# Optimization experiments

Measured on AMD Instinct MI355X. Metric: run time of the kernel, lower is better.

Reference implementation:

```python
import jax, jax.numpy as jnp
import numpy as np

N, E, D, H, G, C = 100000, 1200000, 64, 64, 128, 10


def setup_inputs() -> dict:
    key = jax.random.key(0)
    ks = jax.random.split(key, 20)
    def lin(k, fin, fout):
        kw, kb = jax.random.split(k)
        s = 1.0 / np.sqrt(fin)
        return (jax.random.uniform(kw, (fin, fout), jnp.float32, -s, s),
                jax.random.uniform(kb, (fout,), jnp.float32, -s, s))
    w1a, b1a = lin(ks[0], D, H)
    w1b, b1b = lin(ks[1], H, H)
    w2a, b2a = lin(ks[2], H, H)
    w2b, b2b = lin(ks[3], H, H)
    w3a, b3a = lin(ks[4], H, H)
    w3b, b3b = lin(ks[5], H, H)
    wc, bc = lin(ks[6], H, C)
    x = jax.random.normal(ks[7], (N, D), jnp.float32)
    edge_index = jax.random.randint(ks[8], (2, E), 0, N, dtype=jnp.int32)
    batch = jnp.sort(jax.random.randint(ks[9], (N,), 0, G, dtype=jnp.int32))
    return {"x": x, "w1a": w1a, "b1a": b1a, "w1b": w1b, "b1b": b1b,
            "w2a": w2a, "b2a": b2a, "w2b": w2b, "b2b": b2b,
            "w3a": w3a, "b3a": b3a, "w3b": w3b, "b3b": b3b,
            "wc": wc, "bc": bc, "edge_index": edge_index, "batch": batch}


def _gin_layer(x, src, dst, wa, ba, wb, bb):
    # GINConv (eps=0): mlp(x + sum_{j in N(i)} x_j), then outer ReLU from GIN.forward
    agg = jax.ops.segment_sum(x[src], dst, num_segments=N)  # [N, d]
    h = x + agg
    h = jax.nn.relu(h @ wa + ba) @ wb + bb
    return jax.nn.relu(h)


def reference(x, w1a, b1a, w1b, b1b, w2a, b2a, w2b, b2b,
              w3a, b3a, w3b, b3b, wc, bc, edge_index, batch):
    src, dst = edge_index[0], edge_index[1]
    x = _gin_layer(x, src, dst, w1a, b1a, w1b, b1b)
    x = _gin_layer(x, src, dst, w2a, b2a, w2b, b2b)
    x = _gin_layer(x, src, dst, w3a, b3a, w3b, b3b)
    # global mean pool over graphs
    sums = jax.ops.segment_sum(x, batch, num_segments=G)              # [G, H]
    cnts = jax.ops.segment_sum(jnp.ones((N,), x.dtype), batch, num_segments=G)
    pooled = sums / jnp.maximum(cnts, 1.0)[:, None]
    return pooled @ wc + bc  # [G, C]
```

## Files before the change

### kernel.cpp

```cpp
#include <hip/hip_runtime.h>
#include <hip/hip_bf16.h>


#define N_NODES 100000
#define N_EDGES 1200000
#define N_GRAPH 128
#define N_CLS   10
#define NBUCK   391
#define BCAP    4096
#define BSH     12

typedef __bf16 bf16_t;
typedef __bf16 bf16x8 __attribute__((ext_vector_type(8)));
typedef float  f32x4  __attribute__((ext_vector_type(4)));

__global__ void tobf_kernel(const float* __restrict__ x, bf16_t* __restrict__ xb,
                            int* __restrict__ bcnt, float* __restrict__ gsum,
                            const float* __restrict__ w1a, const float* __restrict__ w1b,
                            const float* __restrict__ w2a, const float* __restrict__ w2b,
                            const float* __restrict__ w3a, const float* __restrict__ w3b,
                            bf16_t* __restrict__ wfragG,
                            bf16_t* __restrict__ hPad, bf16_t* __restrict__ xAPad) {
    const int tid = threadIdx.x;
    if (blockIdx.x == 0) {
        for (int i = tid; i < NBUCK; i += 256) bcnt[i] = 0;
    } else if (blockIdx.x == 1) {
        f32x4* g4 = (f32x4*)gsum;
        for (int i = tid; i < N_GRAPH * 16; i += 256)
            g4[i] = (f32x4){0.f, 0.f, 0.f, 0.f};
        if (tid < 64) {
            xb[N_NODES * 64 + tid]    = (bf16_t)0.f;
            hPad[N_NODES * 64 + tid]  = (bf16_t)0.f;
            xAPad[N_NODES * 64 + tid] = (bf16_t)0.f;
        }
    } else if (blockIdx.x <= 4) {
        const int L = blockIdx.x - 2;
        const float* wA = L == 0 ? w1a : (L == 1 ? w2a : w3a);
        const float* wB = L == 0 ? w1b : (L == 1 ? w2b : w3b);
        const int k  = tid >> 2;
        const int n0 = (tid & 3) << 4;
        const int ks = k >> 5, qd = (k >> 3) & 3, jj = k & 7;
        const int fi = ((n0 >> 4) << 1) + ks;
#pragma unroll
        for (int m = 0; m < 2; ++m) {
            const float* w = m ? wB : wA;
            const f32x4 v0 = *(const f32x4*)(w + k * 64 + n0);
            const f32x4 v1 = *(const f32x4*)(w + k * 64 + n0 + 4);
            const f32x4 v2 = *(const f32x4*)(w + k * 64 + n0 + 8);
            const f32x4 v3 = *(const f32x4*)(w + k * 64 + n0 + 12);
            bf16_t* dst = wfragG + ((L * 2 + m) * 8 + fi) * 512 + jj;
#pragma unroll
            for (int l = 0; l < 4; ++l) {
                dst[(qd * 16 + l) * 8]      = (bf16_t)v0[l];
                dst[(qd * 16 + 4 + l) * 8]  = (bf16_t)v1[l];
                dst[(qd * 16 + 8 + l) * 8]  = (bf16_t)v2[l];
                dst[(qd * 16 + 12 + l) * 8] = (bf16_t)v3[l];
            }
        }
    }
    const int i = (blockIdx.x * 256 + tid) * 8;
    const f32x4 a = *(const f32x4*)(x + i);
    const f32x4 b = *(const f32x4*)(x + i + 4);
    bf16x8 o;
#pragma unroll
    for (int j = 0; j < 4; ++j) { o[j] = (bf16_t)a[j]; o[4 + j] = (bf16_t)b[j]; }
    *(bf16x8*)(xb + i) = o;
}

__global__ void binA_kernel(const int* __restrict__ ei,
                            int* __restrict__ bcnt,
                            int* __restrict__ bpair) {
    __shared__ int lcnt[NBUCK];
    __shared__ int lbase[NBUCK];
    const int t = threadIdx.x;
    for (int b = t; b < NBUCK; b += 256) lcnt[b] = 0;
    __syncthreads();
    const int e0 = (blockIdx.x * 256 + t) * 4;
    int4 s4, d4; int b[4], r[4];
    const bool valid = e0 < N_EDGES;
    if (valid) {
        s4 = *(const int4*)(ei + e0);
        d4 = *(const int4*)(ei + N_EDGES + e0);
        b[0] = d4.x >> 8; b[1] = d4.y >> 8; b[2] = d4.z >> 8; b[3] = d4.w >> 8;
        r[0] = atomicAdd(&lcnt[b[0]], 1);
        r[1] = atomicAdd(&lcnt[b[1]], 1);
        r[2] = atomicAdd(&lcnt[b[2]], 1);
        r[3] = atomicAdd(&lcnt[b[3]], 1);
    }
    __syncthreads();
    for (int bb = t; bb < NBUCK; bb += 256) {
        const int c = lcnt[bb];
        lbase[bb] = c ? atomicAdd(&bcnt[bb], c) : 0;
    }
    __syncthreads();
    if (valid) {
        const int ss[4] = {s4.x, s4.y, s4.z, s4.w};
        const int dd[4] = {d4.x, d4.y, d4.z, d4.w};
#pragma unroll
        for (int j = 0; j < 4; ++j) {
            const int slot = lbase[b[j]] + r[j];
            if (slot < BCAP)
                bpair[(b[j] << BSH) + slot] = (ss[j] << 8) | (dd[j] & 255);
        }
    }
}

__global__ void sortfill_kernel(const int* __restrict__ bpair,
                                const int* __restrict__ bcnt,
                                int* __restrict__ offset, int* __restrict__ csr) {
    __shared__ int red[256];
    __shared__ int hist[256];
    __shared__ int l[256];
    __shared__ int cursor[256];
    const int b = blockIdx.x;
    const int t = threadIdx.x;
    const int base = b << BSH;

    int part = 0;
    for (int i = t; i < b; i += 256) {
        int c = bcnt[i];
        part += (c < BCAP ? c : BCAP);
    }
    red[t] = part;
    __syncthreads();
    for (int d = 128; d > 0; d >>= 1) {
        if (t < d) red[t] += red[t + d];
        __syncthreads();
    }
    const int cbase = red[0];
    int cnt = bcnt[b];
    cnt = cnt < BCAP ? cnt : BCAP;
    if (b == NBUCK - 1 && t == 0) offset[N_NODES] = cbase + cnt;
    __syncthreads();

    hist[t] = 0;
    __syncthreads();
    for (int i = t; i < cnt; i += 256)
        atomicAdd(&hist[bpair[base + i] & 255], 1);
    __syncthreads();

    const int v = hist[t];
    l[t] = v;
    __syncthreads();
    for (int d = 1; d < 256; d <<= 1) {
        int u = l[t];
        if (t >= d) u += l[t - d];
        __syncthreads();
        l[t] = u;
        __syncthreads();
    }
    const int gpos = cbase + l[t] - v;
    const int node = (b << 8) + t;
    if (node < N_NODES) offset[node] = gpos;
    cursor[t] = gpos;
    __syncthreads();

    for (int i = t; i < cnt; i += 256) {
        const int p = bpair[base + i];
        const int pos = atomicAdd(&cursor[p & 255], 1);
        csr[pos] = p >> 8;
    }
}

#define G8(S, J, ACC)                                                          \
    {                                                                          \
        const int t0 = __shfl(S, (J) + 0), t1 = __shfl(S, (J) + 1);            \
        const int t2 = __shfl(S, (J) + 2), t3 = __shfl(S, (J) + 3);            \
        const int t4 = __shfl(S, (J) + 4), t5 = __shfl(S, (J) + 5);            \
        const int t6 = __shfl(S, (J) + 6), t7 = __shfl(S, (J) + 7);            \
        const float u0 = (float)x[t0 * 64 + f], u1 = (float)x[t1 * 64 + f];    \
        const float u2 = (float)x[t2 * 64 + f], u3 = (float)x[t3 * 64 + f];    \
        const float u4 = (float)x[t4 * 64 + f], u5 = (float)x[t5 * 64 + f];    \
        const float u6 = (float)x[t6 * 64 + f], u7 = (float)x[t7 * 64 + f];    \
        ACC += ((u0 + u1) + (u2 + u3)) + ((u4 + u5) + (u6 + u7));              \
    }

#define ROWPAIR(I, SA, CA, DA, OA, SB, CB, DB, OB)                             \
    {                                                                          \
        float accA = (float)x[(r0w + I) * 64 + f];                             \
        float accB = (float)x[(r0w + I + 4) * 64 + f];                         \
        const int cmax = (CA) > (CB) ? (CA) : (CB);                            \
        for (int j = 0; j < cmax; j += 8) {                                    \
            if (j < (CA)) { G8(SA, j, accA) }                                  \
            if (j < (CB)) { G8(SB, j, accB) }                                  \
        }                                                                      \
        if ((DA) > 64 || (DB) > 64) {                      \
            for (int base = 64; base < (DA) || base < (DB); base += 64) {      \
                const int ra = (DA) - base, rb2 = (DB) - base;                 \
                const int ca2 = ra <= 0 ? 0 : (ra < 64 ? ra : 64);             \
                const int cb2 = rb2 <= 0 ? 0 : (rb2 < 64 ? rb2 : 64);          \
                int sA2 = N_NODES, sB2 = N_NODES;                              \
                if (f < ca2) sA2 = csr[(OA) + base + f];                       \
                if (f < cb2) sB2 = csr[(OB) + base + f];                       \
                const int cm2 = ca2 > cb2 ? ca2 : cb2;                         \
                for (int j = 0; j < cm2; j += 8) {                             \
                    if (j < ca2) { G8(sA2, j, accA) }                          \
                    if (j < cb2) { G8(sB2, j, accB) }                          \
                }                                                              \
            }                                                                  \
        }                                                                      \
        hs[half * 8 + I][lane]     = (bf16_t)accA;                             \
        hs[half * 8 + I + 4][lane] = (bf16_t)accB;                             \
    }

template <int POOL>
__global__ void gmlp_kernel(const bf16_t* __restrict__ x,
                            const int* __restrict__ offset,
                            const int* __restrict__ csr,
                            const bf16_t* __restrict__ wf,
                            const float* __restrict__ ba, const float* __restrict__ bb,
                            bf16_t* __restrict__ xout,
                            const int* __restrict__ batch,
                            float* __restrict__ gsum) {
    __shared__ __align__(16) bf16_t hs[16][72];
    __shared__ __align__(16) bf16_t h2[16][72];

    const int tid  = threadIdx.x;
    const int half = tid >> 6;
    const int lane = tid & 63;
    const int l15  = lane & 15;
    const int quad = lane >> 4;

    const int rb  = blockIdx.x * 16;
    const int r0w = rb + half * 8;
    const int f   = lane;

    int offv = 0;
    if (lane < 9) offv = offset[r0w + lane];
    const int o0 = __shfl(offv, 0), o1 = __shfl(offv, 1), o2 = __shfl(offv, 2);
    const int o3 = __shfl(offv, 3), o4 = __shfl(offv, 4), o5 = __shfl(offv, 5);
    const int o6 = __shfl(offv, 6), o7 = __shfl(offv, 7), o8 = __shfl(offv, 8);
    const int d0 = o1 - o0, d1 = o2 - o1, d2 = o3 - o2, d3 = o4 - o3;
    const int d4 = o5 - o4, d5 = o6 - o5, d6 = o7 - o6, d7 = o8 - o7;
    const int c0 = d0 < 64 ? d0 : 64, c1 = d1 < 64 ? d1 : 64;
    const int c2 = d2 < 64 ? d2 : 64, c3 = d3 < 64 ? d3 : 64;
    const int c4 = d4 < 64 ? d4 : 64, c5 = d5 < 64 ? d5 : 64;
    const int c6 = d6 < 64 ? d6 : 64, c7 = d7 < 64 ? d7 : 64;

    int s0 = N_NODES, s1 = N_NODES, s2 = N_NODES, s3 = N_NODES;
    int s4 = N_NODES, s5 = N_NODES, s6 = N_NODES, s7 = N_NODES;
    if (f < c0) s0 = csr[o0 + f];
    if (f < c1) s1 = csr[o1 + f];
    if (f < c2) s2 = csr[o2 + f];
    if (f < c3) s3 = csr[o3 + f];
    if (f < c4) s4 = csr[o4 + f];
    if (f < c5) s5 = csr[o5 + f];
    if (f < c6) s6 = csr[o6 + f];
    if (f < c7) s7 = csr[o7 + f];

    ROWPAIR(0, s0, c0, d0, o0, s4, c4, d4, o4)
    ROWPAIR(1, s1, c1, d1, o1, s5, c5, d5, o5)
    ROWPAIR(2, s2, c2, d2, o2, s6, c6, d6, o6)
    ROWPAIR(3, s3, c3, d3, o3, s7, c7, d7, o7)

    __syncthreads();

    {
        bf16x8 af[2];
#pragma unroll
        for (int ks = 0; ks < 2; ++ks)
            af[ks] = *(const bf16x8*)(&hs[l15][ks * 32 + quad * 8]);
#pragma unroll
        for (int c = 0; c < 2; ++c) {
            const int ct = half * 2 + c;
            const bf16x8 b0 = *(const bf16x8*)(wf + (0 * 8 + ct * 2 + 0) * 512 + lane * 8);
            const bf16x8 b1 = *(const bf16x8*)(wf + (0 * 8 + ct * 2 + 1) * 512 + lane * 8);
            f32x4 acc = {0.f, 0.f, 0.f, 0.f};
            acc = __builtin_amdgcn_mfma_f32_16x16x32_bf16(af[0], b0, acc, 0, 0, 0);
            acc = __builtin_amdgcn_mfma_f32_16x16x32_bf16(af[1], b1, acc, 0, 0, 0);
            const float bv = ba[ct * 16 + l15];
#pragma unroll
            for (int r = 0; r < 4; ++r) {
                float h = acc[r] + bv;
                h = h > 0.f ? h : 0.f;
                h2[quad * 4 + r][ct * 16 + l15] = (bf16_t)h;
            }
        }
    }

    __syncthreads();

    {
        bf16x8 a2[2];
#pragma unroll
        for (int ks = 0; ks < 2; ++ks)
            a2[ks] = *(const bf16x8*)(&h2[l15][ks * 32 + quad * 8]);
#pragma unroll
        for (int c = 0; c < 2; ++c) {
            const int ct = half * 2 + c;
            const bf16x8 b0 = *(const bf16x8*)(wf + (1 * 8 + ct * 2 + 0) * 512 + lane * 8);
            const bf16x8 b1 = *(const bf16x8*)(wf + (1 * 8 + ct * 2 + 1) * 512 + lane * 8);
            f32x4 acc = {0.f, 0.f, 0.f, 0.f};
            acc = __builtin_amdgcn_mfma_f32_16x16x32_bf16(a2[0], b0, acc, 0, 0, 0);
            acc = __builtin_amdgcn_mfma_f32_16x16x32_bf16(a2[1], b1, acc, 0, 0, 0);
            const float bv = bb[ct * 16 + l15];
#pragma unroll
            for (int r = 0; r < 4; ++r) {
                float h = acc[r] + bv;
                h = h > 0.f ? h : 0.f;
                hs[quad * 4 + r][ct * 16 + l15] = (bf16_t)h;
            }
        }
    }

    __syncthreads();

    if (POOL) {
        int cur = -1;
        float acc = 0.f;
        for (int r = 0; r < 8; ++r) {
            const int row = r0w + r;
            const int g = batch[row];
            const float v = (float)hs[half * 8 + r][lane];
            if (g != cur) {
                if (cur >= 0) unsafeAtomicAdd(gsum + cur * 64 + lane, acc);
                acc = 0.f;
                cur = g;
            }
            acc += v;
        }
        if (cur >= 0) unsafeAtomicAdd(gsum + cur * 64 + lane, acc);
    } else {
        const int row16 = half * 8 + (lane >> 3);
        const int colg  = (lane & 7) * 8;
        const bf16x8 v = *(const bf16x8*)&hs[row16][colg];
        *(bf16x8*)(xout + (rb + row16) * 64 + colg) = v;
    }
}

__global__ void cls_kernel(const float* __restrict__ gsum,
                           const int* __restrict__ batch,
                           const float* __restrict__ wc, const float* __restrict__ bc,
                           float* __restrict__ out) {
    const int g = blockIdx.x;
    const int c = threadIdx.x;
    if (c >= N_CLS) return;
    int lo = 0, hi = N_NODES;
    while (lo < hi) { const int m = (lo + hi) >> 1; if (batch[m] < g) lo = m + 1; else hi = m; }
    const int lb = lo;
    lo = 0; hi = N_NODES;
    while (lo < hi) { const int m = (lo + hi) >> 1; if (batch[m] <= g) lo = m + 1; else hi = m; }
    const int cnt = lo - lb;
    const float inv = 1.f / (float)(cnt > 1 ? cnt : 1);
    float acc = bc[c];
    for (int k = 0; k < 64; ++k)
        acc += gsum[g * 64 + k] * inv * wc[k * N_CLS + c];
    out[g * N_CLS + c] = acc;
}

extern "C" void kernel_launch(void* const* d_in, const int* in_sizes, int n_in,
                              void* d_out, int out_size, void* d_ws, size_t ws_size,
                              hipStream_t stream) {
    const float* x   = (const float*)d_in[0];
    const float* w1a = (const float*)d_in[1];
    const float* b1a = (const float*)d_in[2];
    const float* w1b = (const float*)d_in[3];
    const float* b1b = (const float*)d_in[4];
    const float* w2a = (const float*)d_in[5];
    const float* b2a = (const float*)d_in[6];
    const float* w2b = (const float*)d_in[7];
    const float* b2b = (const float*)d_in[8];
    const float* w3a = (const float*)d_in[9];
    const float* b3a = (const float*)d_in[10];
    const float* w3b = (const float*)d_in[11];
    const float* b3b = (const float*)d_in[12];
    const float* wc  = (const float*)d_in[13];
    const float* bc  = (const float*)d_in[14];
    const int*   ei    = (const int*)d_in[15];
    const int*   batch = (const int*)d_in[16];
    float* out = (float*)d_out;

    char*   ws     = (char*)d_ws;
    int*    bcnt   = (int*)ws;
    int*    offset = (int*)(ws + 3136);
    int*    csr    = (int*)(ws + 403152);
    int*    bpair  = (int*)(ws + 5203152);
    bf16_t* xbf    = (bf16_t*)(ws + 11609296);
    bf16_t* h      = (bf16_t*)(ws + 24409424);
    bf16_t* xA     = (bf16_t*)(ws + 37209552);
    float*  gsum   = (float*)(ws + 50009680);
    bf16_t* wfragG = (bf16_t*)(ws + 50042448);

    const int e4grid = (N_EDGES / 4 + 255) / 256;
    const int tiles  = N_NODES / 16;

    tobf_kernel<<<(N_NODES * 64) / (256 * 8), 256, 0, stream>>>(
        x, xbf, bcnt, gsum, w1a, w1b, w2a, w2b, w3a, w3b, wfragG, h, xA);

    binA_kernel<<<e4grid, 256, 0, stream>>>(ei, bcnt, bpair);
    sortfill_kernel<<<NBUCK, 256, 0, stream>>>(bpair, bcnt, offset, csr);

    gmlp_kernel<0><<<tiles, 128, 0, stream>>>(xbf, offset, csr, wfragG,         b1a, b1b, xA, nullptr, nullptr);
    gmlp_kernel<0><<<tiles, 128, 0, stream>>>(xA,  offset, csr, wfragG + 8192,  b2a, b2b, h,  nullptr, nullptr);
    gmlp_kernel<1><<<tiles, 128, 0, stream>>>(h,   offset, csr, wfragG + 16384, b3a, b3b, nullptr, batch, gsum);

    cls_kernel<<<N_GRAPH, 64, 0, stream>>>(gsum, batch, wc, bc, out);
}
```

Measured before the change: 287.7 us.

## Process two 16-row tiles per block and prefetch second tile's CSR during GEMMs

Each gmlp block now handles 32 rows as two sequential 16-row tiles. The second tile's offsets and first-chunk CSR neighbor indices are loaded while the first tile's MLP GEMMs run, so that index-load latency overlaps compute. The grid is halved, which reduces parallelism and occupancy slack for latency hiding, and the preloaded indices add register pressure.

New measurement: 329.3 us. 14.4% more time.

```diff
diff --git a/kernel.cpp b/kernel.cpp
--- a/kernel.cpp
+++ b/kernel.cpp
@@ -175,23 +175,40 @@
         ACC += ((u0 + u1) + (u2 + u3)) + ((u4 + u5) + (u6 + u7));              \
     }
 
-#define ROWPAIR(I, SA, CA, DA, OA, SB, CB, DB, OB)                             \
+#define PRELOAD1(OV, X, SX)                                                    \
     {                                                                          \
-        float accA = (float)x[(r0w + I) * 64 + f];                             \
-        float accB = (float)x[(r0w + I + 4) * 64 + f];                         \
-        const int cmax = (CA) > (CB) ? (CA) : (CB);                            \
+        const int o_ = __shfl(OV, X);                                          \
+        const int d_ = __shfl(OV, (X) + 1) - o_;                               \
+        const int c_ = d_ < 64 ? d_ : 64;                                      \
+        SX = N_NODES;                                                          \
+        if (f < c_) SX = csr[o_ + f];                                          \
+    }
+#define PRELOAD8(OV, S0_, S1_, S2_, S3_, S4_, S5_, S6_, S7_)                   \
+    PRELOAD1(OV, 0, S0_) PRELOAD1(OV, 1, S1_) PRELOAD1(OV, 2, S2_)             \
+    PRELOAD1(OV, 3, S3_) PRELOAD1(OV, 4, S4_) PRELOAD1(OV, 5, S5_)             \
+    PRELOAD1(OV, 6, S6_) PRELOAD1(OV, 7, S7_)
+
+#define ROWPAIR(I, OV, SA, SB, R0W)                                            \
+    {                                                                          \
+        const int oA = __shfl(OV, I),     eA = __shfl(OV, (I) + 1);            \
+        const int oB = __shfl(OV, (I) + 4), eB = __shfl(OV, (I) + 5);          \
+        const int dA = eA - oA, dB = eB - oB;                                  \
+        const int cA = dA < 64 ? dA : 64, cB = dB < 64 ? dB : 64;              \
+        float accA = (float)x[((R0W) + I) * 64 + f];                           \
+        float accB = (float)x[((R0W) + I + 4) * 64 + f];                       \
+        const int cmax = cA > cB ? cA : cB;                                    \
         for (int j = 0; j < cmax; j += 8) {                                    \
-            if (j < (CA)) { G8(SA, j, accA) }                                  \
-            if (j < (CB)) { G8(SB, j, accB) }                                  \
+            if (j < cA) { G8(SA, j, accA) }                                    \
+            if (j < cB) { G8(SB, j, accB) }                                    \
         }                                                                      \
-        if ((DA) > 64 || (DB) > 64) {                      \
-            for (int base = 64; base < (DA) || base < (DB); base += 64) {      \
-                const int ra = (DA) - base, rb2 = (DB) - base;                 \
+        if (dA > 64 || dB > 64) {                          \
+            for (int base = 64; base < dA || base < dB; base += 64) {          \
+                const int ra = dA - base, rb2 = dB - base;                     \
                 const int ca2 = ra <= 0 ? 0 : (ra < 64 ? ra : 64);             \
                 const int cb2 = rb2 <= 0 ? 0 : (rb2 < 64 ? rb2 : 64);          \
                 int sA2 = N_NODES, sB2 = N_NODES;                              \
-                if (f < ca2) sA2 = csr[(OA) + base + f];                       \
-                if (f < cb2) sB2 = csr[(OB) + base + f];                       \
+                if (f < ca2) sA2 = csr[oA + base + f];                         \
+                if (f < cb2) sB2 = csr[oB + base + f];                         \
                 const int cm2 = ca2 > cb2 ? ca2 : cb2;                         \
                 for (int j = 0; j < cm2; j += 8) {                             \
                     if (j < ca2) { G8(sA2, j, accA) }                          \
@@ -201,6 +218,77 @@
         }                                                                      \
         hs[half * 8 + I][lane]     = (bf16_t)accA;                             \
         hs[half * 8 + I + 4][lane] = (bf16_t)accB;                             \
+    }
+
+#define GEMM1_BODY                                                             \
+    {                                                                          \
+        bf16x8 af[2];                                                          \
+        _Pragma("unroll")                                                      \
+        for (int ks = 0; ks < 2; ++ks)                                         \
+            af[ks] = *(const bf16x8*)(&hs[l15][ks * 32 + quad * 8]);           \
+        _Pragma("unroll")                                                      \
+        for (int c = 0; c < 2; ++c) {                                          \
+            const int ct = half * 2 + c;                                       \
+            const bf16x8 b0 = *(const bf16x8*)(wf + (ct * 2 + 0) * 512 + lane * 8); \
+            const bf16x8 b1 = *(const bf16x8*)(wf + (ct * 2 + 1) * 512 + lane * 8); \
+            f32x4 acc = {0.f, 0.f, 0.f, 0.f};                                  \
+            acc = __builtin_amdgcn_mfma_f32_16x16x32_bf16(af[0], b0, acc, 0, 0, 0); \
+            acc = __builtin_amdgcn_mfma_f32_16x16x32_bf16(af[1], b1, acc, 0, 0, 0); \
+            const float bv = ba[ct * 16 + l15];                                \
+            _Pragma("unroll")                                                  \
+            for (int r = 0; r < 4; ++r) {                                      \
+                float h = acc[r] + bv;                                         \
+                h = h > 0.f ? h : 0.f;                                         \
+                h2[quad * 4 + r][ct * 16 + l15] = (bf16_t)h;                   \
+            }                                                                  \
+        }                                                                      \
+    }
+
+#define GEMM2_BODY                                                             \
+    {                                                                          \
+        bf16x8 a2[2];                                                          \
+        _Pragma("unroll")                                                      \
+        for (int ks = 0; ks < 2; ++ks)                                         \
+            a2[ks] = *(const bf16x8*)(&h2[l15][ks * 32 + quad * 8]);           \
+        _Pragma("unroll")                                                      \
+        for (int c = 0; c < 2; ++c) {                                          \
+            const int ct = half * 2 + c;                                       \
+            const bf16x8 b0 = *(const bf16x8*)(wf + (8 + ct * 2 + 0) * 512 + lane * 8); \
+            const bf16x8 b1 = *(const bf16x8*)(wf + (8 + ct * 2 + 1) * 512 + lane * 8); \
+            f32x4 acc = {0.f, 0.f, 0.f, 0.f};                                  \
+            acc = __builtin_amdgcn_mfma_f32_16x16x32_bf16(a2[0], b0, acc, 0, 0, 0); \
+            acc = __builtin_amdgcn_mfma_f32_16x16x32_bf16(a2[1], b1, acc, 0, 0, 0); \
+            const float bv = bb[ct * 16 + l15];                                \
+            _Pragma("unroll")                                                  \
+            for (int r = 0; r < 4; ++r) {                                      \
+                float h = acc[r] + bv;                                         \
+                h = h > 0.f ? h : 0.f;                                         \
+                hs[quad * 4 + r][ct * 16 + l15] = (bf16_t)h;                   \
+            }                                                                  \
+        }                                                                      \
+    }
+
+#define EPILOGUE(RB, R0W)                                                      \
+    if (POOL) {                                                                \
+        int cur = -1;                                                          \
+        float acc = 0.f;                                                       \
+        for (int r = 0; r < 8; ++r) {                                          \
+            const int row = (R0W) + r;                                         \
+            const int g = batch[row];                        \
+            const float v = (float)hs[half * 8 + r][lane];                     \
+            if (g != cur) {                                                    \
+                if (cur >= 0) unsafeAtomicAdd(gsum + cur * 64 + lane, acc);    \
+                acc = 0.f;                                                     \
+                cur = g;                                                       \
+            }                                                                  \
+            acc += v;                                                          \
+        }                                                                      \
+        if (cur >= 0) unsafeAtomicAdd(gsum + cur * 64 + lane, acc);            \
+    } else {                                                                   \
+        const int row16 = half * 8 + (lane >> 3);                              \
+        const int colg  = (lane & 7) * 8;                                      \
+        const bf16x8 v = *(const bf16x8*)&hs[row16][colg];                     \
+        *(bf16x8*)(xout + ((RB) + row16) * 64 + colg) = v;                     \
     }
 
 template <int POOL>
@@ -220,112 +308,50 @@
     const int lane = tid & 63;
     const int l15  = lane & 15;
     const int quad = lane >> 4;
-
-    const int rb  = blockIdx.x * 16;
-    const int r0w = rb + half * 8;
-    const int f   = lane;
-
-    int offv = 0;
-    if (lane < 9) offv = offset[r0w + lane];
-    const int o0 = __shfl(offv, 0), o1 = __shfl(offv, 1), o2 = __shfl(offv, 2);
-    const int o3 = __shfl(offv, 3), o4 = __shfl(offv, 4), o5 = __shfl(offv, 5);
-    const int o6 = __shfl(offv, 6), o7 = __shfl(offv, 7), o8 = __shfl(offv, 8);
-    const int d0 = o1 - o0, d1 = o2 - o1, d2 = o3 - o2, d3 = o4 - o3;
-    const int d4 = o5 - o4, d5 = o6 - o5, d6 = o7 - o6, d7 = o8 - o7;
-    const int c0 = d0 < 64 ? d0 : 64, c1 = d1 < 64 ? d1 : 64;
-    const int c2 = d2 < 64 ? d2 : 64, c3 = d3 < 64 ? d3 : 64;
-    const int c4 = d4 < 64 ? d4 : 64, c5 = d5 < 64 ? d5 : 64;
-    const int c6 = d6 < 64 ? d6 : 64, c7 = d7 < 64 ? d7 : 64;
-
-    int s0 = N_NODES, s1 = N_NODES, s2 = N_NODES, s3 = N_NODES;
-    int s4 = N_NODES, s5 = N_NODES, s6 = N_NODES, s7 = N_NODES;
-    if (f < c0) s0 = csr[o0 + f];
-    if (f < c1) s1 = csr[o1 + f];
-    if (f < c2) s2 = csr[o2 + f];
-    if (f < c3) s3 = csr[o3 + f];
-    if (f < c4) s4 = csr[o4 + f];
-    if (f < c5) s5 = csr[o5 + f];
-    if (f < c6) s6 = csr[o6 + f];
-    if (f < c7) s7 = csr[o7 + f];
-
-    ROWPAIR(0, s0, c0, d0, o0, s4, c4, d4, o4)
-    ROWPAIR(1, s1, c1, d1, o1, s5, c5, d5, o5)
-    ROWPAIR(2, s2, c2, d2, o2, s6, c6, d6, o6)
-    ROWPAIR(3, s3, c3, d3, o3, s7, c7, d7, o7)
-
-    __syncthreads();
-
-    {
-        bf16x8 af[2];
-#pragma unroll
-        for (int ks = 0; ks < 2; ++ks)
-            af[ks] = *(const bf16x8*)(&hs[l15][ks * 32 + quad * 8]);
-#pragma unroll
-        for (int c = 0; c < 2; ++c) {
-            const int ct = half * 2 + c;
-            const bf16x8 b0 = *(const bf16x8*)(wf + (0 * 8 + ct * 2 + 0) * 512 + lane * 8);
-            const bf16x8 b1 = *(const bf16x8*)(wf + (0 * 8 + ct * 2 + 1) * 512 + lane * 8);
-            f32x4 acc = {0.f, 0.f, 0.f, 0.f};
-            acc = __builtin_amdgcn_mfma_f32_16x16x32_bf16(af[0], b0, acc, 0, 0, 0);
-            acc = __builtin_amdgcn_mfma_f32_16x16x32_bf16(af[1], b1, acc, 0, 0, 0);
-            const float bv = ba[ct * 16 + l15];
-#pragma unroll
-            for (int r = 0; r < 4; ++r) {
-                float h = acc[r] + bv;
-                h = h > 0.f ? h : 0.f;
-                h2[quad * 4 + r][ct * 16 + l15] = (bf16_t)h;
-            }
-        }
-    }
-
-    __syncthreads();
-
-    {
-        bf16x8 a2[2];
-#pragma unroll
-        for (int ks = 0; ks < 2; ++ks)
-            a2[ks] = *(const bf16x8*)(&h2[l15][ks * 32 + quad * 8]);
-#pragma unroll
-        for (int c = 0; c < 2; ++c) {
-            const int ct = half * 2 + c;
-            const bf16x8 b0 = *(const bf16x8*)(wf + (1 * 8 + ct * 2 + 0) * 512 + lane * 8);
-            const bf16x8 b1 = *(const bf16x8*)(wf + (1 * 8 + ct * 2 + 1) * 512 + lane * 8);
-            f32x4 acc = {0.f, 0.f, 0.f, 0.f};
-            acc = __builtin_amdgcn_mfma_f32_16x16x32_bf16(a2[0], b0, acc, 0, 0, 0);
-            acc = __builtin_amdgcn_mfma_f32_16x16x32_bf16(a2[1], b1, acc, 0, 0, 0);
-            const float bv = bb[ct * 16 + l15];
-#pragma unroll
-            for (int r = 0; r < 4; ++r) {
-                float h = acc[r] + bv;
-                h = h > 0.f ? h : 0.f;
-                hs[quad * 4 + r][ct * 16 + l15] = (bf16_t)h;
-            }
-        }
-    }
-
-    __syncthreads();
-
-    if (POOL) {
-        int cur = -1;
-        float acc = 0.f;
-        for (int r = 0; r < 8; ++r) {
-            const int row = r0w + r;
-            const int g = batch[row];
-            const float v = (float)hs[half * 8 + r][lane];
-            if (g != cur) {
-                if (cur >= 0) unsafeAtomicAdd(gsum + cur * 64 + lane, acc);
-                acc = 0.f;
-                cur = g;
-            }
-            acc += v;
-        }
-        if (cur >= 0) unsafeAtomicAdd(gsum + cur * 64 + lane, acc);
-    } else {
-        const int row16 = half * 8 + (lane >> 3);
-        const int colg  = (lane & 7) * 8;
-        const bf16x8 v = *(const bf16x8*)&hs[row16][colg];
-        *(bf16x8*)(xout + (rb + row16) * 64 + colg) = v;
-    }
+    const int f    = lane;
+
+    const int rb0  = blockIdx.x * 32;
+    const int rb1  = rb0 + 16;
+    const int r0wA = rb0 + half * 8;
+    const int r0wB = rb1 + half * 8;
+
+    int offvA = 0;
+    if (lane < 9) offvA = offset[r0wA + lane];
+    int a0, a1, a2, a3, a4, a5, a6, a7;
+    PRELOAD8(offvA, a0, a1, a2, a3, a4, a5, a6, a7)
+
+    ROWPAIR(0, offvA, a0, a4, r0wA)
+    ROWPAIR(1, offvA, a1, a5, r0wA)
+    ROWPAIR(2, offvA, a2, a6, r0wA)
+    ROWPAIR(3, offvA, a3, a7, r0wA)
+
+    int offvB = 0;
+    if (lane < 9) offvB = offset[r0wB + lane];
+
+    __syncthreads();
+    GEMM1_BODY
+
+    int b0_, b1_, b2_, b3_, b4_, b5_, b6_, b7_;
+    PRELOAD8(offvB, b0_, b1_, b2_, b3_, b4_, b5_, b6_, b7_)
+
+    __syncthreads();
+    GEMM2_BODY
+    __syncthreads();
+    EPILOGUE(rb0, r0wA)
+
+    __syncthreads();
+
+    ROWPAIR(0, offvB, b0_, b4_, r0wB)
+    ROWPAIR(1, offvB, b1_, b5_, r0wB)
+    ROWPAIR(2, offvB, b2_, b6_, r0wB)
+    ROWPAIR(3, offvB, b3_, b7_, r0wB)
+
+    __syncthreads();
+    GEMM1_BODY
+    __syncthreads();
+    GEMM2_BODY
+    __syncthreads();
+    EPILOGUE(rb1, r0wB)
 }
 
 __global__ void cls_kernel(const float* __restrict__ gsum,
@@ -382,7 +408,7 @@
     bf16_t* wfragG = (bf16_t*)(ws + 50042448);
 
     const int e4grid = (N_EDGES / 4 + 255) / 256;
-    const int tiles  = N_NODES / 16;
+    const int tiles2 = N_NODES / 32;
 
     tobf_kernel<<<(N_NODES * 64) / (256 * 8), 256, 0, stream>>>(
         x, xbf, bcnt, gsum, w1a, w1b, w2a, w2b, w3a, w3b, wfragG, h, xA);
@@ -390,9 +416,9 @@
     binA_kernel<<<e4grid, 256, 0, stream>>>(ei, bcnt, bpair);
     sortfill_kernel<<<NBUCK, 256, 0, stream>>>(bpair, bcnt, offset, csr);
 
-    gmlp_kernel<0><<<tiles, 128, 0, stream>>>(xbf, offset, csr, wfragG,         b1a, b1b, xA, nullptr, nullptr);
-    gmlp_kernel<0><<<tiles, 128, 0, stream>>>(xA,  offset, csr, wfragG + 8192,  b2a, b2b, h,  nullptr, nullptr);
-    gmlp_kernel<1><<<tiles, 128, 0, stream>>>(h,   offset, csr, wfragG + 16384, b3a, b3b, nullptr, batch, gsum);
+    gmlp_kernel<0><<<tiles2, 128, 0, stream>>>(xbf, offset, csr, wfragG,         b1a, b1b, xA, nullptr, nullptr);
+    gmlp_kernel<0><<<tiles2, 128, 0, stream>>>(xA,  offset, csr, wfragG + 8192,  b2a, b2b, h,  nullptr, nullptr);
+    gmlp_kernel<1><<<tiles2, 128, 0, stream>>>(h,   offset, csr, wfragG + 16384, b3a, b3b, nullptr, batch, gsum);
 
     cls_kernel<<<N_GRAPH, 64, 0, stream>>>(gsum, batch, wc, bc, out);
 }
```
